# Optimization experiments

Hardware: AMD Instinct MI355X
Metric: run time of the kernel (lower is better)

The kernel has to match this reference:

```python
import jax, jax.numpy as jnp
import numpy as np

B, N, E = 2, 4096, 768
H = 12
HD = E // H  # 64

def setup_inputs() -> dict:
    key = jax.random.key(0)
    k1, k2, k3, k4, k5 = jax.random.split(key, 5)
    s = 0.02
    return {
        "x": jax.random.normal(k1, (B, N, E), dtype=jnp.float32),
        "w_qkv": jax.random.normal(k2, (3 * E, E), dtype=jnp.float32) * s,
        "b_qkv": jax.random.normal(k3, (3 * E,), dtype=jnp.float32) * s,
        "w_proj": jax.random.normal(k4, (E, E), dtype=jnp.float32) * s,
        "b_proj": jax.random.normal(k5, (E,), dtype=jnp.float32) * s,
    }

def reference(x, w_qkv, b_qkv, w_proj, b_proj):
    b, n, e = x.shape
    hd = e // H
    # fused QKV projection (torch Linear: x @ W.T + b)
    qkv = jnp.einsum('bne,fe->bnf', x, w_qkv) + b_qkv          # [B,N,3E]
    # faithful to torch reshape(B,N,H,3*hd).permute(0,2,1,3).chunk(3,-1)
    qkv = qkv.reshape(b, n, H, 3 * hd).transpose(0, 2, 1, 3)    # [B,H,N,3hd]
    q, k, v = jnp.split(qkv, 3, axis=-1)                        # each [B,H,N,hd]
    attn = jnp.einsum('bhqd,bhkd->bhqk', q, k) / jnp.sqrt(jnp.float32(hd))
    attn = jax.nn.softmax(attn, axis=-1)                        # [B,H,N,N]
    # dropout layers are identity in eval mode
    out = jnp.einsum('bhqk,bhkd->bhqd', attn, v)                # [B,H,N,hd]
    out = out.transpose(0, 2, 1, 3).reshape(b, n, e)            # [B,N,E]
    out = jnp.einsum('bne,fe->bnf', out, w_proj) + b_proj
    return out
```

## Files before the change

kernel.cpp:

```cpp
#include <hip/hip_runtime.h>

typedef unsigned short u16;
typedef __bf16 bf16x8 __attribute__((ext_vector_type(8)));
typedef float f32x4 __attribute__((ext_vector_type(4)));
typedef unsigned short u16x8 __attribute__((ext_vector_type(8)));

__device__ __forceinline__ u16 f2bf(float f) {
    __bf16 h = (__bf16)f;
    union { __bf16 h; u16 u; } cv; cv.h = h;
    return cv.u;
}

__device__ __forceinline__ f32x4 mfma16(bf16x8 a, bf16x8 b, f32x4 c) {
    return __builtin_amdgcn_mfma_f32_16x16x32_bf16(a, b, c, 0, 0, 0);
}

__device__ __forceinline__ void gll16(const u16* gp, u16* lp) {
    __builtin_amdgcn_global_load_lds(
        (__attribute__((address_space(1))) void*)const_cast<u16*>(gp),
        (__attribute__((address_space(3))) void*)lp,
        16, 0, 0);
}

__global__ __launch_bounds__(256) void cvt_bf16(const float* __restrict__ in,
                                                u16* __restrict__ out) {
    int i = blockIdx.x * 256 + threadIdx.x;
    const float4* p = (const float4*)in;
    float4 a = p[2 * i];
    float4 b = p[2 * i + 1];
    u16x8 r;
    r[0] = f2bf(a.x); r[1] = f2bf(a.y); r[2] = f2bf(a.z); r[3] = f2bf(a.w);
    r[4] = f2bf(b.x); r[5] = f2bf(b.y); r[6] = f2bf(b.z); r[7] = f2bf(b.w);
    *(u16x8*)&out[8 * i] = r;
}

__global__ __launch_bounds__(256) void gemm_qkv(
    const u16* __restrict__ A, const u16* __restrict__ W,
    const float* __restrict__ bias,
    u16* __restrict__ Qg, u16* __restrict__ Kg, u16* __restrict__ Vtg)
{
    __shared__ __attribute__((aligned(16))) u16 As[128 * 32];
    __shared__ __attribute__((aligned(16))) u16 Bs[128 * 32];
    const int tid = threadIdx.x;
    const int lane = tid & 63, wave = tid >> 6;
    const int lo = lane & 15, hi = lane >> 4;
    const int wm = (wave >> 1) * 64, wn = (wave & 1) * 64;
    const int m0 = blockIdx.y * 128, n0 = blockIdx.x * 128;

    f32x4 acc[4][4];
#pragma unroll
    for (int i = 0; i < 4; i++)
#pragma unroll
        for (int j = 0; j < 4; j++) acc[i][j] = f32x4{0.f, 0.f, 0.f, 0.f};

    const int ar = tid >> 2, ac = (tid & 3) * 8;
    const u16* ga = A + (size_t)(m0 + ar) * 768 + ac;
    const u16* gb = W + (size_t)(n0 + ar) * 768 + ac;

    for (int kt = 0; kt < 768; kt += 32) {
        gll16(ga + kt,            &As[tid * 8]);
        gll16(ga + kt + 64 * 768, &As[2048 + tid * 8]);
        gll16(gb + kt,            &Bs[tid * 8]);
        gll16(gb + kt + 64 * 768, &Bs[2048 + tid * 8]);
        __syncthreads();
        bf16x8 af[4], bfr[4];
#pragma unroll
        for (int mi = 0; mi < 4; mi++)
            af[mi] = *(const bf16x8*)&As[(wm + mi * 16 + lo) * 32 + hi * 8];
#pragma unroll
        for (int ni = 0; ni < 4; ni++)
            bfr[ni] = *(const bf16x8*)&Bs[(wn + ni * 16 + lo) * 32 + hi * 8];
#pragma unroll
        for (int mi = 0; mi < 4; mi++)
#pragma unroll
            for (int ni = 0; ni < 4; ni++)
                acc[mi][ni] = mfma16(af[mi], bfr[ni], acc[mi][ni]);
        __syncthreads();
    }

#pragma unroll
    for (int ni = 0; ni < 4; ni++) {
        const int n = n0 + wn + ni * 16 + lo;
        const int h = n / 192;
        const int rem = n - h * 192;
        const int sel = rem >> 6;
        const int d = rem & 63;
        const float bv = bias[n];
#pragma unroll
        for (int mi = 0; mi < 4; mi++) {
#pragma unroll
            for (int r = 0; r < 4; r++) {
                const int m = m0 + wm + mi * 16 + hi * 4 + r;
                const int bb = m >> 12;
                const int q = m & 4095;
                const float v = acc[mi][ni][r] + bv;
                const size_t bh = (size_t)(bb * 12 + h);
                if (sel == 0) {
                    Qg[(bh * 4096 + q) * 64 + d] = f2bf(v * 0.18033688011112042f);
                } else if (sel == 1) {
                    Kg[(bh * 4096 + q) * 64 + (d ^ ((q & 7) * 8))] = f2bf(v);
                } else {
                    Vtg[(bh * 64 + d) * 4096 +
                        ((q & ~63) | ((q & 63) ^ ((d & 7) * 8)))] = f2bf(v);
                }
            }
        }
    }
}

__global__ __launch_bounds__(256) void attn_kernel(
    const u16* __restrict__ Qg, const u16* __restrict__ Kg,
    const u16* __restrict__ Vtg, u16* __restrict__ Ob)
{
    __shared__ __attribute__((aligned(16))) u16 Ks[128 * 64];
    __shared__ __attribute__((aligned(16))) u16 Vt[64 * 128];
    __shared__ __attribute__((aligned(16))) u16 Ps[4][16 * 64];
    const int tid = threadIdx.x;
    const int lane = tid & 63, wave = tid >> 6;
    const int lo = lane & 15, hi = lane >> 4;
    const int qt = blockIdx.x, h = blockIdx.y, b = blockIdx.z;
    const size_t bh = (size_t)(b * 12 + h);

    bf16x8 qf[2];
    {
        const int qrow = qt * 64 + wave * 16 + lo;
        const u16* qp = Qg + (bh * 4096 + qrow) * 64 + hi * 8;
        qf[0] = *(const bf16x8*)qp;
        qf[1] = *(const bf16x8*)(qp + 32);
    }
    f32x4 o[4];
#pragma unroll
    for (int i = 0; i < 4; i++) o[i] = f32x4{0.f, 0.f, 0.f, 0.f};
    float lp[4] = {0.f, 0.f, 0.f, 0.f};

    const u16* gk = Kg + (bh * 4096 + (tid >> 3)) * 64 + (tid & 7) * 8;
    const u16* gv = Vtg + (bh * 64 + (tid >> 4)) * 4096 + (tid & 15) * 8;
    const int swl = (lo & 7) * 8;

    for (int kt = 0; kt < 4096; kt += 128) {
#pragma unroll
        for (int c = 0; c < 4; c++)
            gll16(gk + (size_t)(kt + c * 32) * 64, &Ks[c * 2048 + tid * 8]);
#pragma unroll
        for (int c = 0; c < 4; c++)
            gll16(gv + kt + (size_t)c * 16 * 4096, &Vt[c * 2048 + tid * 8]);
        __syncthreads();

#pragma unroll
        for (int half = 0; half < 2; half++) {
            f32x4 s[4];
#pragma unroll
            for (int ni = 0; ni < 4; ni++) {
                f32x4 a = f32x4{0.f, 0.f, 0.f, 0.f};
                const int row = half * 64 + ni * 16 + lo;
                a = mfma16(qf[0], *(const bf16x8*)&Ks[row * 64 + ((hi * 8) ^ swl)], a);
                a = mfma16(qf[1], *(const bf16x8*)&Ks[row * 64 + ((32 + hi * 8) ^ swl)], a);
                s[ni] = a;
            }
#pragma unroll
            for (int ni = 0; ni < 4; ni++)
#pragma unroll
                for (int r = 0; r < 4; r++) {
                    const float p = __builtin_amdgcn_exp2f(s[ni][r]);
                    s[ni][r] = p;
                    lp[r] += p;
                }
#pragma unroll
            for (int r = 0; r < 4; r++) {
                const int row = hi * 4 + r;
                const int sw = (row & 7) * 8;
#pragma unroll
                for (int ni = 0; ni < 4; ni++)
                    Ps[wave][row * 64 + ((ni * 16 + lo) ^ sw)] = f2bf(s[ni][r]);
            }
            bf16x8 pf[2];
            pf[0] = *(const bf16x8*)&Ps[wave][lo * 64 + ((hi * 8) ^ swl)];
            pf[1] = *(const bf16x8*)&Ps[wave][lo * 64 + ((32 + hi * 8) ^ swl)];

#pragma unroll
            for (int di = 0; di < 4; di++) {
                const int row = di * 16 + lo;
                const int base = row * 128 + half * 64;
                o[di] = mfma16(pf[0], *(const bf16x8*)&Vt[base + ((hi * 8) ^ swl)], o[di]);
                o[di] = mfma16(pf[1], *(const bf16x8*)&Vt[base + ((32 + hi * 8) ^ swl)], o[di]);
            }
        }
        __syncthreads();
    }

#pragma unroll
    for (int r = 0; r < 4; r++) {
#pragma unroll
        for (int off = 1; off < 16; off <<= 1)
            lp[r] += __shfl_xor(lp[r], off, 64);
    }

#pragma unroll
    for (int r = 0; r < 4; r++) {
        const float inv = 1.f / lp[r];
        const int q = qt * 64 + wave * 16 + hi * 4 + r;
        u16* op = Ob + ((size_t)b * 4096 + q) * 768 + h * 64 + lo;
#pragma unroll
        for (int di = 0; di < 4; di++)
            op[di * 16] = f2bf(o[di][r] * inv);
    }
}

__global__ __launch_bounds__(256) void gemm_proj(
    const u16* __restrict__ A, const u16* __restrict__ W,
    const float* __restrict__ bias, float* __restrict__ C)
{
    __shared__ __attribute__((aligned(16))) u16 As[128 * 32];
    __shared__ __attribute__((aligned(16))) u16 Bs[128 * 32];
    const int tid = threadIdx.x;
    const int lane = tid & 63, wave = tid >> 6;
    const int lo = lane & 15, hi = lane >> 4;
    const int wm = (wave >> 1) * 64, wn = (wave & 1) * 64;
    const int m0 = blockIdx.y * 128, n0 = blockIdx.x * 128;

    f32x4 acc[4][4];
#pragma unroll
    for (int i = 0; i < 4; i++)
#pragma unroll
        for (int j = 0; j < 4; j++) acc[i][j] = f32x4{0.f, 0.f, 0.f, 0.f};

    const int ar = tid >> 2, ac = (tid & 3) * 8;
    const u16* ga = A + (size_t)(m0 + ar) * 768 + ac;
    const u16* gb = W + (size_t)(n0 + ar) * 768 + ac;

    for (int kt = 0; kt < 768; kt += 32) {
        gll16(ga + kt,            &As[tid * 8]);
        gll16(ga + kt + 64 * 768, &As[2048 + tid * 8]);
        gll16(gb + kt,            &Bs[tid * 8]);
        gll16(gb + kt + 64 * 768, &Bs[2048 + tid * 8]);
        __syncthreads();
        bf16x8 af[4], bfr[4];
#pragma unroll
        for (int mi = 0; mi < 4; mi++)
            af[mi] = *(const bf16x8*)&As[(wm + mi * 16 + lo) * 32 + hi * 8];
#pragma unroll
        for (int ni = 0; ni < 4; ni++)
            bfr[ni] = *(const bf16x8*)&Bs[(wn + ni * 16 + lo) * 32 + hi * 8];
#pragma unroll
        for (int mi = 0; mi < 4; mi++)
#pragma unroll
            for (int ni = 0; ni < 4; ni++)
                acc[mi][ni] = mfma16(af[mi], bfr[ni], acc[mi][ni]);
        __syncthreads();
    }

#pragma unroll
    for (int ni = 0; ni < 4; ni++) {
        const int n = n0 + wn + ni * 16 + lo;
        const float bv = bias[n];
#pragma unroll
        for (int mi = 0; mi < 4; mi++) {
#pragma unroll
            for (int r = 0; r < 4; r++) {
                const int m = m0 + wm + mi * 16 + hi * 4 + r;
                C[(size_t)m * 768 + n] = acc[mi][ni][r] + bv;
            }
        }
    }
}

extern "C" void kernel_launch(void* const* d_in, const int* in_sizes, int n_in,
                              void* d_out, int out_size, void* d_ws, size_t ws_size,
                              hipStream_t stream)
{
    const float* x      = (const float*)d_in[0];
    const float* w_qkv  = (const float*)d_in[1];
    const float* b_qkv  = (const float*)d_in[2];
    const float* w_proj = (const float*)d_in[3];
    const float* b_proj = (const float*)d_in[4];
    float* out = (float*)d_out;

    u16* ws  = (u16*)d_ws;
    u16* xb  = ws;
    u16* wqb = xb + 6291456;
    u16* wpb = wqb + 1769472;
    u16* Qg  = wpb + 589824;
    u16* Kg  = Qg + 6291456;
    u16* Vtg = Kg + 6291456;
    u16* Ob  = Vtg + 6291456;

    cvt_bf16<<<3072, 256, 0, stream>>>(x, xb);
    cvt_bf16<<<864,  256, 0, stream>>>(w_qkv, wqb);
    cvt_bf16<<<288,  256, 0, stream>>>(w_proj, wpb);
    gemm_qkv<<<dim3(18, 64), 256, 0, stream>>>(xb, wqb, b_qkv, Qg, Kg, Vtg);
    attn_kernel<<<dim3(64, 12, 2), 256, 0, stream>>>(Qg, Kg, Vtg, Ob);
    gemm_proj<<<dim3(6, 64), 256, 0, stream>>>(Ob, wpb, b_proj, out);
}
```

Before: 340.2 us.

## Process 32 query rows per wave in attention to reuse K/V fragments

Each wave now computes two 16-row query tiles, so every K and V fragment loaded from LDS feeds two MFMAs, and the block covers 128 queries, halving global K/V reloads. QK^T is computed with K as the A operand so each lane holds four consecutive keys, allowing vectorised P stores to LDS and a cheaper row-sum reduction. The cost is higher register pressure, a doubled P buffer, and half as many blocks, which may reduce occupancy.

```diff
diff --git a/kernel.cpp b/kernel.cpp
--- a/kernel.cpp
+++ b/kernel.cpp
@@ -4,6 +4,7 @@
 typedef __bf16 bf16x8 __attribute__((ext_vector_type(8)));
 typedef float f32x4 __attribute__((ext_vector_type(4)));
 typedef unsigned short u16x8 __attribute__((ext_vector_type(8)));
+typedef unsigned short u16x4 __attribute__((ext_vector_type(4)));
 
 __device__ __forceinline__ u16 f2bf(float f) {
     __bf16 h = (__bf16)f;
@@ -108,34 +109,37 @@
     }
 }
 
-__global__ __launch_bounds__(256) void attn_kernel(
+__global__ __launch_bounds__(256, 3) void attn_kernel(
     const u16* __restrict__ Qg, const u16* __restrict__ Kg,
     const u16* __restrict__ Vtg, u16* __restrict__ Ob)
 {
     __shared__ __attribute__((aligned(16))) u16 Ks[128 * 64];
     __shared__ __attribute__((aligned(16))) u16 Vt[64 * 128];
-    __shared__ __attribute__((aligned(16))) u16 Ps[4][16 * 64];
+    __shared__ __attribute__((aligned(16))) u16 Ps[8][16 * 64];
     const int tid = threadIdx.x;
     const int lane = tid & 63, wave = tid >> 6;
     const int lo = lane & 15, hi = lane >> 4;
     const int qt = blockIdx.x, h = blockIdx.y, b = blockIdx.z;
     const size_t bh = (size_t)(b * 12 + h);
-
-    bf16x8 qf[2];
-    {
-        const int qrow = qt * 64 + wave * 16 + lo;
+    const int swl = (lo & 7) * 8;
+
+    bf16x8 qf[2][2];
+#pragma unroll
+    for (int t = 0; t < 2; t++) {
+        const int qrow = qt * 128 + wave * 32 + t * 16 + lo;
         const u16* qp = Qg + (bh * 4096 + qrow) * 64 + hi * 8;
-        qf[0] = *(const bf16x8*)qp;
-        qf[1] = *(const bf16x8*)(qp + 32);
-    }
-    f32x4 o[4];
-#pragma unroll
-    for (int i = 0; i < 4; i++) o[i] = f32x4{0.f, 0.f, 0.f, 0.f};
-    float lp[4] = {0.f, 0.f, 0.f, 0.f};
+        qf[t][0] = *(const bf16x8*)qp;
+        qf[t][1] = *(const bf16x8*)(qp + 32);
+    }
+    f32x4 o[2][4];
+#pragma unroll
+    for (int t = 0; t < 2; t++)
+#pragma unroll
+        for (int i = 0; i < 4; i++) o[t][i] = f32x4{0.f, 0.f, 0.f, 0.f};
+    float lp[2] = {0.f, 0.f};
 
     const u16* gk = Kg + (bh * 4096 + (tid >> 3)) * 64 + (tid & 7) * 8;
     const u16* gv = Vtg + (bh * 64 + (tid >> 4)) * 4096 + (tid & 15) * 8;
-    const int swl = (lo & 7) * 8;
 
     for (int kt = 0; kt < 4096; kt += 128) {
 #pragma unroll
@@ -148,61 +152,73 @@
 
 #pragma unroll
         for (int half = 0; half < 2; half++) {
-            f32x4 s[4];
+            f32x4 st[2][4];
 #pragma unroll
             for (int ni = 0; ni < 4; ni++) {
-                f32x4 a = f32x4{0.f, 0.f, 0.f, 0.f};
                 const int row = half * 64 + ni * 16 + lo;
-                a = mfma16(qf[0], *(const bf16x8*)&Ks[row * 64 + ((hi * 8) ^ swl)], a);
-                a = mfma16(qf[1], *(const bf16x8*)&Ks[row * 64 + ((32 + hi * 8) ^ swl)], a);
-                s[ni] = a;
-            }
-#pragma unroll
-            for (int ni = 0; ni < 4; ni++)
-#pragma unroll
-                for (int r = 0; r < 4; r++) {
-                    const float p = __builtin_amdgcn_exp2f(s[ni][r]);
-                    s[ni][r] = p;
-                    lp[r] += p;
+                const bf16x8 kf0 = *(const bf16x8*)&Ks[row * 64 + ((hi * 8) ^ swl)];
+                const bf16x8 kf1 = *(const bf16x8*)&Ks[row * 64 + ((32 + hi * 8) ^ swl)];
+                st[0][ni] = mfma16(kf0, qf[0][0], f32x4{0.f, 0.f, 0.f, 0.f});
+                st[0][ni] = mfma16(kf1, qf[0][1], st[0][ni]);
+                st[1][ni] = mfma16(kf0, qf[1][0], f32x4{0.f, 0.f, 0.f, 0.f});
+                st[1][ni] = mfma16(kf1, qf[1][1], st[1][ni]);
+            }
+#pragma unroll
+            for (int t = 0; t < 2; t++) {
+#pragma unroll
+                for (int ni = 0; ni < 4; ni++) {
+                    u16x4 w;
+#pragma unroll
+                    for (int r = 0; r < 4; r++) {
+                        const float p = __builtin_amdgcn_exp2f(st[t][ni][r]);
+                        lp[t] += p;
+                        w[r] = f2bf(p);
+                    }
+                    *(u16x4*)&Ps[wave * 2 + t]
+                        [lo * 64 + ((ni * 16 + hi * 4) ^ swl)] = w;
                 }
-#pragma unroll
-            for (int r = 0; r < 4; r++) {
-                const int row = hi * 4 + r;
-                const int sw = (row & 7) * 8;
-#pragma unroll
-                for (int ni = 0; ni < 4; ni++)
-                    Ps[wave][row * 64 + ((ni * 16 + lo) ^ sw)] = f2bf(s[ni][r]);
-            }
-            bf16x8 pf[2];
-            pf[0] = *(const bf16x8*)&Ps[wave][lo * 64 + ((hi * 8) ^ swl)];
-            pf[1] = *(const bf16x8*)&Ps[wave][lo * 64 + ((32 + hi * 8) ^ swl)];
+            }
+            bf16x8 pf[2][2];
+#pragma unroll
+            for (int t = 0; t < 2; t++)
+#pragma unroll
+                for (int p = 0; p < 2; p++)
+                    pf[t][p] = *(const bf16x8*)&Ps[wave * 2 + t]
+                        [lo * 64 + ((p * 32 + hi * 8) ^ swl)];
 
 #pragma unroll
             for (int di = 0; di < 4; di++) {
-                const int row = di * 16 + lo;
-                const int base = row * 128 + half * 64;
-                o[di] = mfma16(pf[0], *(const bf16x8*)&Vt[base + ((hi * 8) ^ swl)], o[di]);
-                o[di] = mfma16(pf[1], *(const bf16x8*)&Vt[base + ((32 + hi * 8) ^ swl)], o[di]);
+                const int base = (di * 16 + lo) * 128 + half * 64;
+#pragma unroll
+                for (int p = 0; p < 2; p++) {
+                    const bf16x8 vt = *(const bf16x8*)
+                        &Vt[base + ((p * 32 + hi * 8) ^ swl)];
+                    o[0][di] = mfma16(pf[0][p], vt, o[0][di]);
+                    o[1][di] = mfma16(pf[1][p], vt, o[1][di]);
+                }
             }
         }
         __syncthreads();
     }
 
 #pragma unroll
-    for (int r = 0; r < 4; r++) {
-#pragma unroll
-        for (int off = 1; off < 16; off <<= 1)
-            lp[r] += __shfl_xor(lp[r], off, 64);
-    }
-
-#pragma unroll
-    for (int r = 0; r < 4; r++) {
-        const float inv = 1.f / lp[r];
-        const int q = qt * 64 + wave * 16 + hi * 4 + r;
-        u16* op = Ob + ((size_t)b * 4096 + q) * 768 + h * 64 + lo;
-#pragma unroll
-        for (int di = 0; di < 4; di++)
-            op[di * 16] = f2bf(o[di][r] * inv);
+    for (int t = 0; t < 2; t++) {
+        lp[t] += __shfl_xor(lp[t], 16, 64);
+        lp[t] += __shfl_xor(lp[t], 32, 64);
+    }
+
+#pragma unroll
+    for (int t = 0; t < 2; t++) {
+#pragma unroll
+        for (int r = 0; r < 4; r++) {
+            const float rs = __shfl(lp[t], hi * 4 + r, 64);
+            const float inv = 1.f / rs;
+            const int q = qt * 128 + wave * 32 + t * 16 + hi * 4 + r;
+            u16* op = Ob + ((size_t)b * 4096 + q) * 768 + h * 64 + lo;
+#pragma unroll
+            for (int di = 0; di < 4; di++)
+                op[di * 16] = f2bf(o[t][di][r] * inv);
+        }
     }
 }
 
@@ -288,6 +304,6 @@
     cvt_bf16<<<864,  256, 0, stream>>>(w_qkv, wqb);
     cvt_bf16<<<288,  256, 0, stream>>>(w_proj, wpb);
     gemm_qkv<<<dim3(18, 64), 256, 0, stream>>>(xb, wqb, b_qkv, Qg, Kg, Vtg);
-    attn_kernel<<<dim3(64, 12, 2), 256, 0, stream>>>(Qg, Kg, Vtg, Ob);
+    attn_kernel<<<dim3(32, 12, 2), 256, 0, stream>>>(Qg, Kg, Vtg, Ob);
     gemm_proj<<<dim3(6, 64), 256, 0, stream>>>(Ob, wpb, b_proj, out);
 }
```

After: 324.9 us. 4.5% less time.
